# Optimization experiments

Hardware: AMD Instinct MI355X
Metric: run time of the kernel (lower is better)

## Reference

```python
import jax, jax.numpy as jnp
import numpy as np

HIDDEN = 1024
H = 16        # num query heads
HKV = 4       # num kv heads
GROUPS = H // HKV
D = HIDDEN // H  # head_dim = 64
SW = (63, 0)  # sliding_window (left, right)
W = SW[0] + SW[1] + 1  # window length per query = 64
MAXPOS = 2048


def _sincos_table(num_pos, dim):
    # faithful to create_sinusoidal_positions (incl. final [:, :, :num_pos] slice)
    inv_freq = 1.0 / 10000 ** (np.arange(0, dim, 2, dtype=np.int32) / dim)
    freqs = np.einsum('i,j->ij', np.arange(num_pos, dtype=np.int32), inv_freq).astype(np.float32)
    emb = np.concatenate((freqs, freqs), axis=-1)
    out = np.concatenate((np.sin(emb)[:, None, :], np.cos(emb)[:, None, :]), axis=-1)
    return jnp.asarray(out[:, :, :num_pos])  # [num_pos, 1, 2*dim]

_SINCOS = _sincos_table(MAXPOS, D)


def _rotate_half(x):
    h = x.shape[-1] // 2
    return jnp.concatenate((-x[..., h:], x[..., :h]), axis=-1)


def setup_inputs() -> dict:
    key = jax.random.key(0)
    k0, k1, k2, k3, k4 = jax.random.split(key, 5)
    B, S = 1, 2048
    std = 0.02
    return {
        'hidden_states': jax.random.normal(k0, (B, S, HIDDEN), dtype=jnp.float32),
        'attention_mask': jnp.ones((B, S, 1, W), dtype=jnp.int32),
        'position_ids': jnp.arange(B * S, dtype=jnp.int32).reshape(B, S) % MAXPOS,
        'q_kernel': jax.random.normal(k1, (HIDDEN, H * D), dtype=jnp.float32) * std,
        'k_kernel': jax.random.normal(k2, (HIDDEN, HKV * D), dtype=jnp.float32) * std,
        'v_kernel': jax.random.normal(k3, (HIDDEN, HKV * D), dtype=jnp.float32) * std,
        'o_kernel': jax.random.normal(k4, (HIDDEN, HIDDEN), dtype=jnp.float32) * std,
    }


def reference(hidden_states, attention_mask, position_ids, q_kernel, k_kernel, v_kernel, o_kernel):
    B, S, _ = hidden_states.shape
    # QKV projections (no bias)
    q = (hidden_states @ q_kernel).reshape(B, S, H, D)
    k = (hidden_states @ k_kernel).reshape(B, S, HKV, D)
    v = (hidden_states @ v_kernel).reshape(B, S, HKV, D)
    # rotary embedding; sincos[pos] -> [B,S,1,2D], broadcasts over head axis
    sc = _SINCOS[position_ids]
    sin, cos = jnp.split(sc, 2, axis=-1)
    k = k * cos + _rotate_half(k) * sin
    q = q * cos + _rotate_half(q) * sin
    # GQA: repeat kv heads to match query heads
    k = jnp.repeat(k, GROUPS, axis=2)  # [B,S,H,D]
    v = jnp.repeat(v, GROUPS, axis=2)
    # sliding-window gather: each query position sees W surrounding keys
    k = jnp.pad(k, ((0, 0), SW, (0, 0), (0, 0)))
    v = jnp.pad(v, ((0, 0), SW, (0, 0), (0, 0)))
    idx = jnp.arange(W, dtype=jnp.int32)[None, :] + jnp.arange(S, dtype=jnp.int32)[:, None]  # [S,W]
    kg = k[:, idx]  # [B,S,W,H,D]
    vg = v[:, idx]
    # attention (q_len=1 per position), scores [B,S,H,W]
    scores = jnp.einsum('bshd,bswhd->bshw', q, kg) / jnp.asarray(np.sqrt(D), scores_dtype := jnp.float32)
    neg = jnp.finfo(jnp.float32).min
    m = attention_mask[:, :, 0, :][:, :, None, :]  # [B,S,1,W] broadcast over H
    bias = jnp.where(m > 0, jnp.float32(0.0), neg)
    weights = jax.nn.softmax(scores + bias, axis=-1)
    attn = jnp.einsum('bshw,bswhd->bshd', weights, vg).reshape(B, S, HIDDEN)
    return attn @ o_kernel
```

## Files before the change

kernel.cpp:

```cpp
#include <hip/hip_runtime.h>
#include <hip/hip_bf16.h>
#include <math.h>

#define S        2048
#define HIDDEN   1024
#define NH       16
#define NKV      4
#define HD       64
#define NQKV     1536
#define VW       2128

typedef _Float16 f16x8 __attribute__((ext_vector_type(8)));
typedef _Float16 f16x4 __attribute__((ext_vector_type(4)));
typedef float    f32x4 __attribute__((ext_vector_type(4)));

__device__ __forceinline__ void glds16(const void* g, void* l) {
    __builtin_amdgcn_global_load_lds((const __attribute__((address_space(1))) void*)g,
                                     (__attribute__((address_space(3))) void*)l, 16, 0, 0);
}

__device__ __host__ __forceinline__ int ropePerm(int d) {
    int t = d & 48;
    return (t == 16 || t == 32) ? (d ^ 48) : d;
}

__global__ __launch_bounds__(256) void prep_kernel(const float* __restrict__ hs, _Float16* __restrict__ hsf16,
                                                   const float* __restrict__ wq, const float* __restrict__ wk,
                                                   const float* __restrict__ wvv, const float* __restrict__ wo,
                                                   _Float16* __restrict__ wqkvT, _Float16* __restrict__ woT,
                                                   const int* __restrict__ pos_ids, float2* __restrict__ rope_tab,
                                                   _Float16* __restrict__ vTs) {
    int bid = blockIdx.x;
    int tid = threadIdx.x;
    if (bid >= 4864) {
        int d = bid - 4864;
        if (tid < 64) vTs[(size_t)d * VW + tid] = (_Float16)0.0f;
        return;
    }
    if (bid >= 4608) {
        int idx = (bid - 4608) * 256 + tid;
        int s = idx >> 5, f = idx & 31;
        double inv = pow(10000.0, -(double)(2 * f) / 64.0);
        float ang = (float)((double)pos_ids[s] * inv);
        float sn, cs;
        sincosf(ang, &sn, &cs);
        rope_tab[idx] = make_float2(sn, cs);
        return;
    }
    if (bid >= 2560) {
        int i = (bid - 2560) * 256 + tid;
        float4 v = ((const float4*)hs)[i];
        f16x4 o = { (_Float16)v.x, (_Float16)v.y, (_Float16)v.z, (_Float16)v.w };
        *(f16x4*)(hsf16 + 4 * (size_t)i) = o;
        return;
    }
    const float* src; _Float16* dst; int Cn, b; bool prm;
    if (bid < 1024)      { src = wq;  dst = wqkvT;                       Cn = 1024; b = bid;        prm = true;  }
    else if (bid < 1280) { src = wk;  dst = wqkvT + (size_t)1024 * 1024; Cn = 256;  b = bid - 1024; prm = true;  }
    else if (bid < 1536) { src = wvv; dst = wqkvT + (size_t)1280 * 1024; Cn = 256;  b = bid - 1280; prm = false; }
    else                 { src = wo;  dst = woT;                         Cn = 1024; b = bid - 1536; prm = false; }
    int xb = Cn >> 5;
    int c0 = (b % xb) * 32;
    int r0 = (b / xb) * 32;
    __shared__ float t[32][33];
    int tx = tid & 31, ty = tid >> 5;
#pragma unroll
    for (int i = ty; i < 32; i += 8)
        t[i][tx] = src[(size_t)(r0 + i) * Cn + c0 + tx];
    __syncthreads();
#pragma unroll
    for (int i = ty; i < 32; i += 8) {
        int n = c0 + i;
        int np = prm ? ((n & ~63) | ropePerm(n & 63)) : n;
        dst[(size_t)np * 1024 + r0 + tx] = (_Float16)t[tx][i];
    }
}

__global__ __launch_bounds__(256) void gemm_qkv(const _Float16* __restrict__ A,
                                                const _Float16* __restrict__ BT,
                                                _Float16* __restrict__ qkv,
                                                _Float16* __restrict__ vTs,
                                                const float2* __restrict__ rope_tab) {
    __shared__ __align__(16) _Float16 As[64 * 64];
    __shared__ __align__(16) _Float16 Bs[64 * 64];
    const int bid  = blockIdx.x;
    const int tid  = threadIdx.x;
    const int lane = tid & 63;
    const int wv   = tid >> 6;
    const int lr   = lane & 15;
    const int quad = lane >> 4;
    const int dr   = lane >> 3;
    const int cc   = lane & 7;
    const int wm   = (wv >> 1) * 32;
    const int wn   = (wv & 1) * 32;
    const int bx = bid % 24, by = bid / 24;
    const int m0 = by * 64, n0 = bx * 64;

    f32x4 acc[2][2] = {};
    for (int k0 = 0; k0 < 1024; k0 += 64) {
        __syncthreads();
#pragma unroll
        for (int u = 0; u < 2; ++u) {
            int r = wv * 16 + u * 8 + dr;
            glds16(A  + (size_t)(m0 + r) * 1024 + k0 + (cc ^ (r & 7)) * 8, As + (wv * 16 + u * 8) * 64);
            glds16(BT + (size_t)(n0 + r) * 1024 + k0 + (cc ^ (r & 7)) * 8, Bs + (wv * 16 + u * 8) * 64);
        }
        __syncthreads();
#pragma unroll
        for (int ks = 0; ks < 2; ++ks) {
            f16x8 a[2], b[2];
#pragma unroll
            for (int i = 0; i < 2; ++i) {
                int row = wm + i * 16 + lr;
                a[i] = *(const f16x8*)&As[row * 64 + ((ks * 4 + quad) ^ (row & 7)) * 8];
            }
#pragma unroll
            for (int j = 0; j < 2; ++j) {
                int row = wn + j * 16 + lr;
                b[j] = *(const f16x8*)&Bs[row * 64 + ((ks * 4 + quad) ^ (row & 7)) * 8];
            }
#pragma unroll
            for (int i = 0; i < 2; ++i)
#pragma unroll
                for (int j = 0; j < 2; ++j)
                    acc[i][j] = __builtin_amdgcn_mfma_f32_16x16x32_f16(a[i], b[j], acc[i][j], 0, 0, 0);
        }
    }
    if (n0 < 1280) {
        const bool isq = (n0 < 1024);
        const int  f   = (wn >> 1) + lr;
#pragma unroll
        for (int i = 0; i < 2; ++i)
#pragma unroll
            for (int r = 0; r < 4; ++r) {
                int s = m0 + wm + i * 16 + quad * 4 + r;
                float2 scv = rope_tab[(size_t)s * 32 + f];
                float lo = acc[i][0][r], hi = acc[i][1][r];
                float nlo = lo * scv.y - hi * scv.x;
                float nhi = hi * scv.y + lo * scv.x;
                if (isq) { nlo *= 0.125f; nhi *= 0.125f; }
                qkv[(size_t)s * NQKV + n0 + wn + lr]      = (_Float16)nlo;
                qkv[(size_t)s * NQKV + n0 + wn + 16 + lr] = (_Float16)nhi;
            }
    } else {
#pragma unroll
        for (int i = 0; i < 2; ++i)
#pragma unroll
            for (int j = 0; j < 2; ++j) {
                int d = n0 - 1280 + wn + j * 16 + lr;
                f16x4 h = { (_Float16)acc[i][j][0], (_Float16)acc[i][j][1],
                            (_Float16)acc[i][j][2], (_Float16)acc[i][j][3] };
                *(f16x4*)(vTs + (size_t)d * VW + 64 + m0 + wm + i * 16 + quad * 4) = h;
            }
    }
}

__global__ __launch_bounds__(256) void attn_mfma(const _Float16* __restrict__ qkv,
                                                 const _Float16* __restrict__ vTs,
                                                 const int* __restrict__ mask,
                                                 _Float16* __restrict__ attn_out) {
    const int s0   = blockIdx.x * 16;
    const int g    = blockIdx.y;
    const int tid  = threadIdx.x;
    const int lane = tid & 63;
    const int wv   = tid >> 6;
    const int h    = g * 4 + wv;
    const int lr   = lane & 15;
    const int quad = lane >> 4;

    __shared__ __align__(16) _Float16 K_lds[80 * 72];
    __shared__ __align__(16) _Float16 Vt_lds[64 * 104];
    __shared__ __align__(16) _Float16 P_lds[4][16 * 104];
    __shared__ int M_lds[1024];

    ((int4*)M_lds)[tid] = ((const int4*)(mask + s0 * 64))[tid];

    for (int c = tid; c < 640; c += 256) {
        int r = c >> 3, cl = c & 7;
        int j = s0 - 64 + r;
        f16x8 val = {};
        if (j >= 0)
            val = *(const f16x8*)(qkv + (size_t)j * NQKV + 1024 + g * 64 + cl * 8);
        *(f16x8*)&K_lds[r * 72 + cl * 8] = val;
    }
    for (int c = tid; c < 64 * 12; c += 256) {
        int d = c / 12, ch = c % 12;
        *(f16x8*)&Vt_lds[d * 104 + ch * 8] =
            *(const f16x8*)(vTs + (size_t)(g * 64 + d) * VW + s0 + ch * 8);
    }
    f16x8 qf[2];
#pragma unroll
    for (int ks = 0; ks < 2; ++ks)
        qf[ks] = *(const f16x8*)(qkv + (size_t)(s0 + lr) * NQKV + h * 64 + ks * 32 + quad * 8);
    __syncthreads();

    f32x4 sc[5];
#pragma unroll
    for (int t = 0; t < 5; ++t) {
        f32x4 a = {};
#pragma unroll
        for (int ks = 0; ks < 2; ++ks) {
            f16x8 kf = *(const f16x8*)&K_lds[(t * 16 + lr) * 72 + ks * 32 + quad * 8];
            a = __builtin_amdgcn_mfma_f32_16x16x32_f16(qf[ks], kf, a, 0, 0, 0);
        }
        sc[t] = a;
    }
#pragma unroll
    for (int t = 0; t < 5; ++t)
#pragma unroll
        for (int r = 0; r < 4; ++r) {
            int qi = quad * 4 + r;
            int w  = t * 16 + lr - 1 - qi;
            bool ok = (w >= 0) && (w < 64) && (M_lds[qi * 64 + (w & 63)] > 0);
            sc[t][r] = ok ? sc[t][r] : -1e30f;
        }
    float pr[5][4];
#pragma unroll
    for (int r = 0; r < 4; ++r) {
        float mx = -1e30f;
#pragma unroll
        for (int t = 0; t < 5; ++t) mx = fmaxf(mx, sc[t][r]);
#pragma unroll
        for (int off = 1; off < 16; off <<= 1) mx = fmaxf(mx, __shfl_xor(mx, off));
        float sum = 0.f;
#pragma unroll
        for (int t = 0; t < 5; ++t) { float e = __expf(sc[t][r] - mx); pr[t][r] = e; sum += e; }
#pragma unroll
        for (int off = 1; off < 16; off <<= 1) sum += __shfl_xor(sum, off);
        float rs = 1.0f / sum;
#pragma unroll
        for (int t = 0; t < 5; ++t) pr[t][r] *= rs;
    }
    _Float16* myP = P_lds[wv];
    {
        f16x4 z = {};
        *(f16x4*)&myP[lr * 104 + 80 + quad * 4] = z;
    }
#pragma unroll
    for (int t = 0; t < 5; ++t)
#pragma unroll
        for (int r = 0; r < 4; ++r)
            myP[(quad * 4 + r) * 104 + t * 16 + lr] = (_Float16)pr[t][r];
    __syncthreads();

    f32x4 oacc[4] = {};
#pragma unroll
    for (int ks = 0; ks < 3; ++ks) {
        f16x8 pf = *(const f16x8*)&myP[lr * 104 + ks * 32 + quad * 8];
#pragma unroll
        for (int t = 0; t < 4; ++t) {
            f16x8 vf = *(const f16x8*)&Vt_lds[(t * 16 + lr) * 104 + ks * 32 + quad * 8];
            oacc[t] = __builtin_amdgcn_mfma_f32_16x16x32_f16(pf, vf, oacc[t], 0, 0, 0);
        }
    }
#pragma unroll
    for (int t = 0; t < 4; ++t)
#pragma unroll
        for (int r = 0; r < 4; ++r)
            attn_out[(size_t)(s0 + quad * 4 + r) * HIDDEN + h * 64 + t * 16 + lr] = (_Float16)oacc[t][r];
}

__global__ __launch_bounds__(256) void gemm_o(const _Float16* __restrict__ A,
                                              const _Float16* __restrict__ BT,
                                              float* __restrict__ out) {
    __shared__ __align__(16) _Float16 As[64 * 64];
    __shared__ __align__(16) _Float16 Bs[64 * 64];
    const int bid  = blockIdx.x;
    const int tid  = threadIdx.x;
    const int lane = tid & 63;
    const int wv   = tid >> 6;
    const int lr   = lane & 15;
    const int quad = lane >> 4;
    const int dr   = lane >> 3;
    const int cc   = lane & 7;
    const int wm   = (wv >> 1) * 32;
    const int wn   = (wv & 1) * 32;
    const int bx = bid % 16, by = bid / 16;
    const int m0 = by * 64, n0 = bx * 64;

    f32x4 acc[2][2] = {};
    for (int k0 = 0; k0 < 1024; k0 += 64) {
        __syncthreads();
#pragma unroll
        for (int u = 0; u < 2; ++u) {
            int r = wv * 16 + u * 8 + dr;
            glds16(A  + (size_t)(m0 + r) * 1024 + k0 + (cc ^ (r & 7)) * 8, As + (wv * 16 + u * 8) * 64);
            glds16(BT + (size_t)(n0 + r) * 1024 + k0 + (cc ^ (r & 7)) * 8, Bs + (wv * 16 + u * 8) * 64);
        }
        __syncthreads();
#pragma unroll
        for (int ks = 0; ks < 2; ++ks) {
            f16x8 a[2], b[2];
#pragma unroll
            for (int i = 0; i < 2; ++i) {
                int row = wm + i * 16 + lr;
                a[i] = *(const f16x8*)&As[row * 64 + ((ks * 4 + quad) ^ (row & 7)) * 8];
            }
#pragma unroll
            for (int j = 0; j < 2; ++j) {
                int row = wn + j * 16 + lr;
                b[j] = *(const f16x8*)&Bs[row * 64 + ((ks * 4 + quad) ^ (row & 7)) * 8];
            }
#pragma unroll
            for (int i = 0; i < 2; ++i)
#pragma unroll
                for (int j = 0; j < 2; ++j)
                    acc[i][j] = __builtin_amdgcn_mfma_f32_16x16x32_f16(a[i], b[j], acc[i][j], 0, 0, 0);
        }
    }
#pragma unroll
    for (int i = 0; i < 2; ++i)
#pragma unroll
        for (int j = 0; j < 2; ++j)
#pragma unroll
            for (int r = 0; r < 4; ++r)
                out[(size_t)(m0 + wm + i * 16 + quad * 4 + r) * 1024 + n0 + wn + j * 16 + lr] = acc[i][j][r];
}

extern "C" void kernel_launch(void* const* d_in, const int* in_sizes, int n_in,
                              void* d_out, int out_size, void* d_ws, size_t ws_size,
                              hipStream_t stream) {
    const float* hs      = (const float*)d_in[0];
    const int*   mask    = (const int*)  d_in[1];
    const int*   pos_ids = (const int*)  d_in[2];
    const float* wq      = (const float*)d_in[3];
    const float* wk      = (const float*)d_in[4];
    const float* wvv     = (const float*)d_in[5];
    const float* wo      = (const float*)d_in[6];
    float* out = (float*)d_out;

    char* ws = (char*)d_ws;
    _Float16* wqkvT   = (_Float16*)(ws + 0);
    _Float16* woT     = (_Float16*)(ws + (3u << 20));
    _Float16* hsf16   = (_Float16*)(ws + (5u << 20));
    _Float16* qkvf16  = (_Float16*)(ws + (9u << 20));
    _Float16* attnf16 = (_Float16*)(ws + (15u << 20));
    _Float16* vTs     = (_Float16*)(ws + (19u << 20));
    float2*   ropeTab = (float2*)  (ws + (21u << 20));

    prep_kernel<<<5120, 256, 0, stream>>>(hs, hsf16, wq, wk, wvv, wo, wqkvT, woT,
                                          pos_ids, ropeTab, vTs);
    gemm_qkv<<<768, 256, 0, stream>>>(hsf16, wqkvT, qkvf16, vTs, ropeTab);
    attn_mfma<<<dim3(S / 16, NKV), 256, 0, stream>>>(qkvf16, vTs, mask, attnf16);
    gemm_o<<<512, 256, 0, stream>>>(attnf16, woT, out);
}
```

Before: 111.1 us.

## Double-buffer GEMM LDS tiles and use two waves with larger per-wave tiles

Both projection GEMMs now keep two LDS buffers per operand and prefetch the next K-slice through global_load_lds while the current slice is multiplied, which drops one barrier per iteration. Blocks shrink from four waves to two, and each wave computes a 32x64 output tile instead of 32x32, so B fragments are reused across more MFMAs. The cost is fewer waves per block to hide latency, twice the LDS per block, and more accumulator registers. The QKV epilogue is reworked so each wave pairs both rotary halves within its own 64-wide tile.

```diff
diff --git a/kernel.cpp b/kernel.cpp
--- a/kernel.cpp
+++ b/kernel.cpp
@@ -76,13 +76,13 @@
     }
 }
 
-__global__ __launch_bounds__(256) void gemm_qkv(const _Float16* __restrict__ A,
+__global__ __launch_bounds__(128) void gemm_qkv(const _Float16* __restrict__ A,
                                                 const _Float16* __restrict__ BT,
                                                 _Float16* __restrict__ qkv,
                                                 _Float16* __restrict__ vTs,
                                                 const float2* __restrict__ rope_tab) {
-    __shared__ __align__(16) _Float16 As[64 * 64];
-    __shared__ __align__(16) _Float16 Bs[64 * 64];
+    __shared__ __align__(16) _Float16 As[2][64 * 64];
+    __shared__ __align__(16) _Float16 Bs[2][64 * 64];
     const int bid  = blockIdx.x;
     const int tid  = threadIdx.x;
     const int lane = tid & 63;
@@ -91,68 +91,146 @@
     const int quad = lane >> 4;
     const int dr   = lane >> 3;
     const int cc   = lane & 7;
-    const int wm   = (wv >> 1) * 32;
-    const int wn   = (wv & 1) * 32;
+    const int wm   = wv * 32;
     const int bx = bid % 24, by = bid / 24;
     const int m0 = by * 64, n0 = bx * 64;
 
-    f32x4 acc[2][2] = {};
-    for (int k0 = 0; k0 < 1024; k0 += 64) {
+    f32x4 acc[2][4] = {};
+
+#pragma unroll
+    for (int t = 0; t < 4; ++t) {
+        int r = wv * 32 + t * 8 + dr;
+        glds16(A  + (size_t)(m0 + r) * 1024 + (cc ^ (r & 7)) * 8, &As[0][(wv * 32 + t * 8) * 64]);
+        glds16(BT + (size_t)(n0 + r) * 1024 + (cc ^ (r & 7)) * 8, &Bs[0][(wv * 32 + t * 8) * 64]);
+    }
+    int p = 0;
+    for (int it = 0; it < 16; ++it) {
         __syncthreads();
-#pragma unroll
-        for (int u = 0; u < 2; ++u) {
-            int r = wv * 16 + u * 8 + dr;
-            glds16(A  + (size_t)(m0 + r) * 1024 + k0 + (cc ^ (r & 7)) * 8, As + (wv * 16 + u * 8) * 64);
-            glds16(BT + (size_t)(n0 + r) * 1024 + k0 + (cc ^ (r & 7)) * 8, Bs + (wv * 16 + u * 8) * 64);
-        }
-        __syncthreads();
+        if (it < 15) {
+            int k0 = (it + 1) * 64;
+#pragma unroll
+            for (int t = 0; t < 4; ++t) {
+                int r = wv * 32 + t * 8 + dr;
+                glds16(A  + (size_t)(m0 + r) * 1024 + k0 + (cc ^ (r & 7)) * 8, &As[p ^ 1][(wv * 32 + t * 8) * 64]);
+                glds16(BT + (size_t)(n0 + r) * 1024 + k0 + (cc ^ (r & 7)) * 8, &Bs[p ^ 1][(wv * 32 + t * 8) * 64]);
+            }
+        }
 #pragma unroll
         for (int ks = 0; ks < 2; ++ks) {
-            f16x8 a[2], b[2];
+            f16x8 a[2], b[4];
 #pragma unroll
             for (int i = 0; i < 2; ++i) {
                 int row = wm + i * 16 + lr;
-                a[i] = *(const f16x8*)&As[row * 64 + ((ks * 4 + quad) ^ (row & 7)) * 8];
-            }
-#pragma unroll
-            for (int j = 0; j < 2; ++j) {
-                int row = wn + j * 16 + lr;
-                b[j] = *(const f16x8*)&Bs[row * 64 + ((ks * 4 + quad) ^ (row & 7)) * 8];
+                a[i] = *(const f16x8*)&As[p][row * 64 + ((ks * 4 + quad) ^ (row & 7)) * 8];
+            }
+#pragma unroll
+            for (int j = 0; j < 4; ++j) {
+                int row = j * 16 + lr;
+                b[j] = *(const f16x8*)&Bs[p][row * 64 + ((ks * 4 + quad) ^ (row & 7)) * 8];
             }
 #pragma unroll
             for (int i = 0; i < 2; ++i)
 #pragma unroll
-                for (int j = 0; j < 2; ++j)
+                for (int j = 0; j < 4; ++j)
                     acc[i][j] = __builtin_amdgcn_mfma_f32_16x16x32_f16(a[i], b[j], acc[i][j], 0, 0, 0);
         }
+        p ^= 1;
     }
     if (n0 < 1280) {
         const bool isq = (n0 < 1024);
-        const int  f   = (wn >> 1) + lr;
 #pragma unroll
         for (int i = 0; i < 2; ++i)
 #pragma unroll
             for (int r = 0; r < 4; ++r) {
                 int s = m0 + wm + i * 16 + quad * 4 + r;
-                float2 scv = rope_tab[(size_t)s * 32 + f];
-                float lo = acc[i][0][r], hi = acc[i][1][r];
-                float nlo = lo * scv.y - hi * scv.x;
-                float nhi = hi * scv.y + lo * scv.x;
-                if (isq) { nlo *= 0.125f; nhi *= 0.125f; }
-                qkv[(size_t)s * NQKV + n0 + wn + lr]      = (_Float16)nlo;
-                qkv[(size_t)s * NQKV + n0 + wn + 16 + lr] = (_Float16)nhi;
+#pragma unroll
+                for (int pp = 0; pp < 2; ++pp) {
+                    float2 scv = rope_tab[(size_t)s * 32 + pp * 16 + lr];
+                    float lo = acc[i][2 * pp][r], hi = acc[i][2 * pp + 1][r];
+                    float nlo = lo * scv.y - hi * scv.x;
+                    float nhi = hi * scv.y + lo * scv.x;
+                    if (isq) { nlo *= 0.125f; nhi *= 0.125f; }
+                    qkv[(size_t)s * NQKV + n0 + pp * 32 + lr]      = (_Float16)nlo;
+                    qkv[(size_t)s * NQKV + n0 + pp * 32 + 16 + lr] = (_Float16)nhi;
+                }
             }
     } else {
 #pragma unroll
         for (int i = 0; i < 2; ++i)
 #pragma unroll
-            for (int j = 0; j < 2; ++j) {
-                int d = n0 - 1280 + wn + j * 16 + lr;
+            for (int j = 0; j < 4; ++j) {
+                int d = n0 - 1280 + j * 16 + lr;
                 f16x4 h = { (_Float16)acc[i][j][0], (_Float16)acc[i][j][1],
                             (_Float16)acc[i][j][2], (_Float16)acc[i][j][3] };
                 *(f16x4*)(vTs + (size_t)d * VW + 64 + m0 + wm + i * 16 + quad * 4) = h;
             }
     }
+}
+
+__global__ __launch_bounds__(128) void gemm_o(const _Float16* __restrict__ A,
+                                              const _Float16* __restrict__ BT,
+                                              float* __restrict__ out) {
+    __shared__ __align__(16) _Float16 As[2][64 * 64];
+    __shared__ __align__(16) _Float16 Bs[2][64 * 64];
+    const int bid  = blockIdx.x;
+    const int tid  = threadIdx.x;
+    const int lane = tid & 63;
+    const int wv   = tid >> 6;
+    const int lr   = lane & 15;
+    const int quad = lane >> 4;
+    const int dr   = lane >> 3;
+    const int cc   = lane & 7;
+    const int wm   = wv * 32;
+    const int bx = bid % 16, by = bid / 16;
+    const int m0 = by * 64, n0 = bx * 64;
+
+    f32x4 acc[2][4] = {};
+#pragma unroll
+    for (int t = 0; t < 4; ++t) {
+        int r = wv * 32 + t * 8 + dr;
+        glds16(A  + (size_t)(m0 + r) * 1024 + (cc ^ (r & 7)) * 8, &As[0][(wv * 32 + t * 8) * 64]);
+        glds16(BT + (size_t)(n0 + r) * 1024 + (cc ^ (r & 7)) * 8, &Bs[0][(wv * 32 + t * 8) * 64]);
+    }
+    int p = 0;
+    for (int it = 0; it < 16; ++it) {
+        __syncthreads();
+        if (it < 15) {
+            int k0 = (it + 1) * 64;
+#pragma unroll
+            for (int t = 0; t < 4; ++t) {
+                int r = wv * 32 + t * 8 + dr;
+                glds16(A  + (size_t)(m0 + r) * 1024 + k0 + (cc ^ (r & 7)) * 8, &As[p ^ 1][(wv * 32 + t * 8) * 64]);
+                glds16(BT + (size_t)(n0 + r) * 1024 + k0 + (cc ^ (r & 7)) * 8, &Bs[p ^ 1][(wv * 32 + t * 8) * 64]);
+            }
+        }
+#pragma unroll
+        for (int ks = 0; ks < 2; ++ks) {
+            f16x8 a[2], b[4];
+#pragma unroll
+            for (int i = 0; i < 2; ++i) {
+                int row = wm + i * 16 + lr;
+                a[i] = *(const f16x8*)&As[p][row * 64 + ((ks * 4 + quad) ^ (row & 7)) * 8];
+            }
+#pragma unroll
+            for (int j = 0; j < 4; ++j) {
+                int row = j * 16 + lr;
+                b[j] = *(const f16x8*)&Bs[p][row * 64 + ((ks * 4 + quad) ^ (row & 7)) * 8];
+            }
+#pragma unroll
+            for (int i = 0; i < 2; ++i)
+#pragma unroll
+                for (int j = 0; j < 4; ++j)
+                    acc[i][j] = __builtin_amdgcn_mfma_f32_16x16x32_f16(a[i], b[j], acc[i][j], 0, 0, 0);
+        }
+        p ^= 1;
+    }
+#pragma unroll
+    for (int i = 0; i < 2; ++i)
+#pragma unroll
+        for (int j = 0; j < 4; ++j)
+#pragma unroll
+            for (int r = 0; r < 4; ++r)
+                out[(size_t)(m0 + wm + i * 16 + quad * 4 + r) * 1024 + n0 + j * 16 + lr] = acc[i][j][r];
 }
 
 __global__ __launch_bounds__(256) void attn_mfma(const _Float16* __restrict__ qkv,
@@ -260,63 +338,6 @@
             attn_out[(size_t)(s0 + quad * 4 + r) * HIDDEN + h * 64 + t * 16 + lr] = (_Float16)oacc[t][r];
 }
 
-__global__ __launch_bounds__(256) void gemm_o(const _Float16* __restrict__ A,
-                                              const _Float16* __restrict__ BT,
-                                              float* __restrict__ out) {
-    __shared__ __align__(16) _Float16 As[64 * 64];
-    __shared__ __align__(16) _Float16 Bs[64 * 64];
-    const int bid  = blockIdx.x;
-    const int tid  = threadIdx.x;
-    const int lane = tid & 63;
-    const int wv   = tid >> 6;
-    const int lr   = lane & 15;
-    const int quad = lane >> 4;
-    const int dr   = lane >> 3;
-    const int cc   = lane & 7;
-    const int wm   = (wv >> 1) * 32;
-    const int wn   = (wv & 1) * 32;
-    const int bx = bid % 16, by = bid / 16;
-    const int m0 = by * 64, n0 = bx * 64;
-
-    f32x4 acc[2][2] = {};
-    for (int k0 = 0; k0 < 1024; k0 += 64) {
-        __syncthreads();
-#pragma unroll
-        for (int u = 0; u < 2; ++u) {
-            int r = wv * 16 + u * 8 + dr;
-            glds16(A  + (size_t)(m0 + r) * 1024 + k0 + (cc ^ (r & 7)) * 8, As + (wv * 16 + u * 8) * 64);
-            glds16(BT + (size_t)(n0 + r) * 1024 + k0 + (cc ^ (r & 7)) * 8, Bs + (wv * 16 + u * 8) * 64);
-        }
-        __syncthreads();
-#pragma unroll
-        for (int ks = 0; ks < 2; ++ks) {
-            f16x8 a[2], b[2];
-#pragma unroll
-            for (int i = 0; i < 2; ++i) {
-                int row = wm + i * 16 + lr;
-                a[i] = *(const f16x8*)&As[row * 64 + ((ks * 4 + quad) ^ (row & 7)) * 8];
-            }
-#pragma unroll
-            for (int j = 0; j < 2; ++j) {
-                int row = wn + j * 16 + lr;
-                b[j] = *(const f16x8*)&Bs[row * 64 + ((ks * 4 + quad) ^ (row & 7)) * 8];
-            }
-#pragma unroll
-            for (int i = 0; i < 2; ++i)
-#pragma unroll
-                for (int j = 0; j < 2; ++j)
-                    acc[i][j] = __builtin_amdgcn_mfma_f32_16x16x32_f16(a[i], b[j], acc[i][j], 0, 0, 0);
-        }
-    }
-#pragma unroll
-    for (int i = 0; i < 2; ++i)
-#pragma unroll
-        for (int j = 0; j < 2; ++j)
-#pragma unroll
-            for (int r = 0; r < 4; ++r)
-                out[(size_t)(m0 + wm + i * 16 + quad * 4 + r) * 1024 + n0 + wn + j * 16 + lr] = acc[i][j][r];
-}
-
 extern "C" void kernel_launch(void* const* d_in, const int* in_sizes, int n_in,
                               void* d_out, int out_size, void* d_ws, size_t ws_size,
                               hipStream_t stream) {
@@ -340,7 +361,7 @@
 
     prep_kernel<<<5120, 256, 0, stream>>>(hs, hsf16, wq, wk, wvv, wo, wqkvT, woT,
                                           pos_ids, ropeTab, vTs);
-    gemm_qkv<<<768, 256, 0, stream>>>(hsf16, wqkvT, qkvf16, vTs, ropeTab);
+    gemm_qkv<<<768, 128, 0, stream>>>(hsf16, wqkvT, qkvf16, vTs, ropeTab);
     attn_mfma<<<dim3(S / 16, NKV), 256, 0, stream>>>(qkvf16, vTs, mask, attnf16);
-    gemm_o<<<512, 256, 0, stream>>>(attnf16, woT, out);
-}
+    gemm_o<<<512, 128, 0, stream>>>(attnf16, woT, out);
+}
```

New measurement: 120.0 us. +8.0%, slower.
